# Kernel optimization log

Measured on AMD Instinct MI355X. Metric: run time of the kernel, lower is better.

## Reference

```python
import jax, jax.numpy as jnp
import numpy as np

D_MODEL = 768
D_STATE = 16
D_CONV = 4
EXPAND = 2
D_INNER = EXPAND * D_MODEL          # 1536
DT_RANK = (D_MODEL + 15) // 16      # 48 (mamba default: ceil(d_model/16))


def setup_inputs() -> dict:
    key = jax.random.key(0)
    ks = jax.random.split(key, 8)
    B, T = 2, 1024
    s = 0.02
    return {
        "x": jax.random.normal(ks[0], (B, T, D_MODEL), jnp.float32),
        "ln_g": jnp.ones((D_MODEL,), jnp.float32),
        "ln_b": jnp.zeros((D_MODEL,), jnp.float32),
        "W_in": jax.random.normal(ks[1], (2 * D_INNER, D_MODEL), jnp.float32) * s,
        "conv_w": jax.random.normal(ks[2], (D_INNER, 1, D_CONV), jnp.float32) * s,
        "conv_b": jnp.zeros((D_INNER,), jnp.float32),
        "W_xproj": jax.random.normal(ks[3], (DT_RANK + 2 * D_STATE, D_INNER), jnp.float32) * s,
        "W_dt": jax.random.normal(ks[4], (D_INNER, DT_RANK), jnp.float32) * s,
        "b_dt": jax.random.normal(ks[5], (D_INNER,), jnp.float32) * s,
        "A_log": jnp.log(jnp.broadcast_to(jnp.arange(1.0, D_STATE + 1.0, dtype=jnp.float32), (D_INNER, D_STATE))),
        "Dp": jnp.ones((D_INNER,), jnp.float32),
        "W_out": jax.random.normal(ks[6], (D_MODEL, D_INNER), jnp.float32) * s,
    }


def _mamba_block(x, ln_g, ln_b, W_in, conv_w, conv_b, W_xproj, W_dt, b_dt, A_log, Dp, W_out):
    B, T, D = x.shape
    # LayerNorm
    mu = x.mean(-1, keepdims=True)
    var = ((x - mu) ** 2).mean(-1, keepdims=True)
    h = (x - mu) * jax.lax.rsqrt(var + 1e-5) * ln_g + ln_b
    # in_proj -> [B,T,2*d_inner], split into x-branch and gate z
    xz = h @ W_in.T
    xs, z = jnp.split(xz, 2, axis=-1)
    # causal depthwise conv over time (pad left d_conv-1), then SiLU
    xc = jax.lax.conv_general_dilated(
        xs.transpose(0, 2, 1), conv_w, (1,), [(D_CONV - 1, 0)],
        dimension_numbers=("NCH", "OIH", "NCH"), feature_group_count=D_INNER)
    xc = jax.nn.silu(xc.transpose(0, 2, 1) + conv_b)  # [B,T,d_inner]
    # x_proj -> dt_rank + 2*d_state
    x_dbl = xc @ W_xproj.T
    dt_r = x_dbl[..., :DT_RANK]
    Bm = x_dbl[..., DT_RANK:DT_RANK + D_STATE]       # [B,T,n]
    Cm = x_dbl[..., DT_RANK + D_STATE:]              # [B,T,n]
    dt = jax.nn.softplus(dt_r @ W_dt.T + b_dt)       # [B,T,d_inner]
    A = -jnp.exp(A_log)                              # [d_inner, n]
    dA = jnp.exp(jnp.einsum("btd,dn->btdn", dt, A))  # [B,T,d,n]
    dBu = jnp.einsum("btd,btn->btdn", dt * xc, Bm)   # [B,T,d,n]

    def step(s, inp):
        dA_t, dBu_t, C_t = inp
        s = dA_t * s + dBu_t                          # [B,d,n]
        y_t = jnp.einsum("bdn,bn->bd", s, C_t)
        return s, y_t

    s0 = jnp.zeros((B, D_INNER, D_STATE), x.dtype)
    _, ys = jax.lax.scan(step, s0,
                         (dA.transpose(1, 0, 2, 3), dBu.transpose(1, 0, 2, 3), Cm.transpose(1, 0, 2)))
    y = ys.transpose(1, 0, 2) + Dp * xc              # D skip connection
    y = y * jax.nn.silu(z)                           # gate
    return x + y @ W_out.T                           # out_proj + residual


def reference(x, ln_g, ln_b, W_in, conv_w, conv_b, W_xproj, W_dt, b_dt, A_log, Dp, W_out):
    return _mamba_block(x, ln_g, ln_b, W_in, conv_w, conv_b, W_xproj, W_dt, b_dt, A_log, Dp, W_out)
```

## Files before the change

### kernel.cpp

```cpp
#include <hip/hip_runtime.h>

typedef unsigned short u16;
typedef unsigned int u32;
typedef __attribute__((ext_vector_type(8))) short short8;
typedef __attribute__((ext_vector_type(4))) float f32x4;

#define D_MODEL 768
#define D_INNER 1536
#define D_XZ    3072
#define D_STATE 16
#define DT_RANK 48
#define NROW    2048
#define SEQ     1024
#define XDS     128
#define NCHUNK  128
#define CLEN    8

typedef const __attribute__((address_space(1))) u32 glb_u32;
typedef __attribute__((address_space(3))) u32 lds_u32;

__device__ __forceinline__ float bf2f(u16 u) {
    union { unsigned int i; float f; } v; v.i = ((unsigned int)u) << 16; return v.f;
}
__device__ __forceinline__ u16 f2bf(float f) {
    union { float f; unsigned int i; } v; v.f = f;
    unsigned int r = v.i + 0x7fffu + ((v.i >> 16) & 1u);
    return (u16)(r >> 16);
}
__device__ __forceinline__ void g2lds16(const u16* g, u16* l) {
    __builtin_amdgcn_global_load_lds((glb_u32*)g, (lds_u32*)l, 16, 0, 0);
}

#define N0 (D_XZ * D_MODEL / 4)
#define N1 (D_MODEL * D_INNER / 4)
#define N2 (XDS * D_INNER / 4)
#define N3 (D_INNER * 64 / 4)
#define N4 (D_INNER * D_STATE / 4)
#define N5 (NROW * XDS / 4)
__global__ __launch_bounds__(256) void prep_weights_k(
    const float* __restrict__ W_in, const float* __restrict__ W_out,
    const float* __restrict__ W_xp, const float* __restrict__ W_dt,
    const float* __restrict__ A_log,
    u16* __restrict__ Win_bf, u16* __restrict__ Wout_bf,
    u16* __restrict__ Wxp_bf, u16* __restrict__ Wdt_bf,
    float* __restrict__ negA, float* __restrict__ xdbl)
{
    int gid = blockIdx.x * 256 + threadIdx.x;
    if (gid < N0) {
        float4 v = *(const float4*)(W_in + (size_t)gid * 4);
        u16* o = Win_bf + (size_t)gid * 4;
        o[0]=f2bf(v.x); o[1]=f2bf(v.y); o[2]=f2bf(v.z); o[3]=f2bf(v.w);
    } else if (gid < N0 + N1) {
        int i = gid - N0;
        float4 v = *(const float4*)(W_out + (size_t)i * 4);
        u16* o = Wout_bf + (size_t)i * 4;
        o[0]=f2bf(v.x); o[1]=f2bf(v.y); o[2]=f2bf(v.z); o[3]=f2bf(v.w);
    } else if (gid < N0 + N1 + N2) {
        int i = gid - N0 - N1;
        int n = (i * 4) / D_INNER, k = (i * 4) % D_INNER;
        u16* o = Wxp_bf + (size_t)i * 4;
        if (n < 80) {
            float4 v = *(const float4*)(W_xp + (size_t)n * D_INNER + k);
            o[0]=f2bf(v.x); o[1]=f2bf(v.y); o[2]=f2bf(v.z); o[3]=f2bf(v.w);
        } else { o[0]=0; o[1]=0; o[2]=0; o[3]=0; }
    } else if (gid < N0 + N1 + N2 + N3) {
        int i = gid - N0 - N1 - N2;
        int r = (i * 4) >> 6, c0 = (i * 4) & 63;
        u16* o = Wdt_bf + (size_t)i * 4;
        if (c0 < DT_RANK) {
            float4 v = *(const float4*)(W_dt + (size_t)r * DT_RANK + c0);
            o[0]=f2bf(v.x); o[1]=f2bf(v.y); o[2]=f2bf(v.z); o[3]=f2bf(v.w);
        } else { o[0]=0; o[1]=0; o[2]=0; o[3]=0; }
    } else if (gid < N0 + N1 + N2 + N3 + N4) {
        int i = gid - N0 - N1 - N2 - N3;
        float4 v = *(const float4*)(A_log + (size_t)i * 4);
        float4 o = make_float4(-__expf(v.x), -__expf(v.y), -__expf(v.z), -__expf(v.w));
        *(float4*)(negA + (size_t)i * 4) = o;
    } else if (gid < N0 + N1 + N2 + N3 + N4 + N5) {
        int i = gid - N0 - N1 - N2 - N3 - N4;
        *(float4*)(xdbl + (size_t)i * 4) = make_float4(0.f, 0.f, 0.f, 0.f);
    }
}

__global__ __launch_bounds__(256) void layernorm_k(
    const float* __restrict__ x, const float* __restrict__ g,
    const float* __restrict__ b, u16* __restrict__ h)
{
    int row = blockIdx.x, tid = threadIdx.x;
    const float* xr = x + (size_t)row * D_MODEL;
    float v[3], s = 0.f, sq = 0.f;
#pragma unroll
    for (int j = 0; j < 3; ++j) {
        v[j] = xr[tid + j * 256];
        s += v[j]; sq += v[j] * v[j];
    }
#pragma unroll
    for (int off = 32; off >= 1; off >>= 1) {
        s  += __shfl_xor(s,  off, 64);
        sq += __shfl_xor(sq, off, 64);
    }
    __shared__ float sred[4], sqred[4];
    if ((tid & 63) == 0) { sred[tid >> 6] = s; sqred[tid >> 6] = sq; }
    __syncthreads();
    float st = sred[0] + sred[1] + sred[2] + sred[3];
    float sqt = sqred[0] + sqred[1] + sqred[2] + sqred[3];
    float mu = st * (1.f / D_MODEL);
    float var = sqt * (1.f / D_MODEL) - mu * mu;
    float rstd = rsqrtf(var + 1e-5f);
    u16* hr = h + (size_t)row * D_MODEL;
#pragma unroll
    for (int j = 0; j < 3; ++j) {
        int idx = tid + j * 256;
        hr[idx] = f2bf((v[j] - mu) * rstd * g[idx] + b[idx]);
    }
}

template<int MT, int NT, bool OUT_BF16, bool ADD_RES>
__global__ __launch_bounds__(256) void gemm128(
    const u16* __restrict__ A, const u16* __restrict__ B,
    const float* __restrict__ Res, void* __restrict__ Cv,
    int M, int N, int K)
{
    constexpr int BM = 32 * MT, BN = 32 * NT;
    __shared__ __align__(16) u16 As[BM * 32];
    __shared__ __align__(16) u16 Bs[BN * 32];
    int tid = threadIdx.x, w = tid >> 6, lane = tid & 63;
    int wm = w & 1, wn = w >> 1;
    int m0 = blockIdx.x * BM, n0 = blockIdx.y * BN;
    int mloc = lane & 15, quad = lane >> 4;
    int lr = lane >> 2, lc = lane & 3;
    f32x4 acc[MT][NT] = {};

    for (int k0 = 0; k0 < K; k0 += 32) {
        __syncthreads();
#pragma unroll
        for (int j = w; j < 2 * MT; j += 4) {
            int row = j * 16 + lr;
            int cb = lc ^ ((row >> 1) & 3);
            g2lds16(A + (size_t)(m0 + row) * K + k0 + cb * 8, &As[j * 512]);
        }
#pragma unroll
        for (int j = w; j < 2 * NT; j += 4) {
            int row = j * 16 + lr;
            int cb = lc ^ ((row >> 1) & 3);
            g2lds16(B + (size_t)(n0 + row) * K + k0 + cb * 8, &Bs[j * 512]);
        }
        __syncthreads();
        short8 afr[MT], bfr[NT];
#pragma unroll
        for (int mt = 0; mt < MT; ++mt) {
            int row = wm * MT * 16 + mt * 16 + mloc;
            int cb = quad ^ ((row >> 1) & 3);
            afr[mt] = *(const short8*)(&As[row * 32 + cb * 8]);
        }
#pragma unroll
        for (int nt = 0; nt < NT; ++nt) {
            int row = wn * NT * 16 + nt * 16 + mloc;
            int cb = quad ^ ((row >> 1) & 3);
            bfr[nt] = *(const short8*)(&Bs[row * 32 + cb * 8]);
        }
#pragma unroll
        for (int mt = 0; mt < MT; ++mt)
#pragma unroll
            for (int nt = 0; nt < NT; ++nt)
                acc[mt][nt] = __builtin_amdgcn_mfma_f32_16x16x32_bf16(
                    afr[mt], bfr[nt], acc[mt][nt], 0, 0, 0);
    }
#pragma unroll
    for (int mt = 0; mt < MT; ++mt) {
        int grow0 = m0 + wm * MT * 16 + mt * 16 + quad * 4;
#pragma unroll
        for (int nt = 0; nt < NT; ++nt) {
            int gcol = n0 + wn * NT * 16 + nt * 16 + mloc;
#pragma unroll
            for (int r = 0; r < 4; ++r) {
                size_t idx = (size_t)(grow0 + r) * N + gcol;
                float v = acc[mt][nt][r];
                if (ADD_RES) v += Res[idx];
                if (OUT_BF16) ((u16*)Cv)[idx] = f2bf(v);
                else          ((float*)Cv)[idx] = v;
            }
        }
    }
}

__global__ __launch_bounds__(256) void xproj_splitk(
    const u16* __restrict__ A, const u16* __restrict__ B, float* __restrict__ Cout)
{
    constexpr int MT = 2, NT = 4;
    __shared__ __align__(16) u16 As[64 * 32];
    __shared__ __align__(16) u16 Bs[128 * 32];
    int tid = threadIdx.x, w = tid >> 6, lane = tid & 63;
    int wm = w & 1, wn = w >> 1;
    int m0 = blockIdx.x * 64;
    int kbase = blockIdx.y * 192;
    int mloc = lane & 15, quad = lane >> 4;
    int lr = lane >> 2, lc = lane & 3;
    f32x4 acc[MT][NT] = {};

    for (int k0 = 0; k0 < 192; k0 += 32) {
        __syncthreads();
#pragma unroll
        for (int j = w; j < 2 * MT; j += 4) {
            int row = j * 16 + lr;
            int cb = lc ^ ((row >> 1) & 3);
            g2lds16(A + (size_t)(m0 + row) * D_INNER + kbase + k0 + cb * 8, &As[j * 512]);
        }
#pragma unroll
        for (int j = w; j < 2 * NT; j += 4) {
            int row = j * 16 + lr;
            int cb = lc ^ ((row >> 1) & 3);
            g2lds16(B + (size_t)row * D_INNER + kbase + k0 + cb * 8, &Bs[j * 512]);
        }
        __syncthreads();
        short8 afr[MT], bfr[NT];
#pragma unroll
        for (int mt = 0; mt < MT; ++mt) {
            int row = wm * MT * 16 + mt * 16 + mloc;
            int cb = quad ^ ((row >> 1) & 3);
            afr[mt] = *(const short8*)(&As[row * 32 + cb * 8]);
        }
#pragma unroll
        for (int nt = 0; nt < NT; ++nt) {
            int row = wn * NT * 16 + nt * 16 + mloc;
            int cb = quad ^ ((row >> 1) & 3);
            bfr[nt] = *(const short8*)(&Bs[row * 32 + cb * 8]);
        }
#pragma unroll
        for (int mt = 0; mt < MT; ++mt)
#pragma unroll
            for (int nt = 0; nt < NT; ++nt)
                acc[mt][nt] = __builtin_amdgcn_mfma_f32_16x16x32_bf16(
                    afr[mt], bfr[nt], acc[mt][nt], 0, 0, 0);
    }
#pragma unroll
    for (int mt = 0; mt < MT; ++mt) {
        int grow0 = m0 + wm * MT * 16 + mt * 16 + quad * 4;
#pragma unroll
        for (int nt = 0; nt < NT; ++nt) {
            int gcol = wn * NT * 16 + nt * 16 + mloc;
#pragma unroll
            for (int r = 0; r < 4; ++r)
                unsafeAtomicAdd(&Cout[(size_t)(grow0 + r) * XDS + gcol], acc[mt][nt][r]);
        }
    }
}

__global__ __launch_bounds__(256) void dtgemm_k(
    const float* __restrict__ xdbl, const u16* __restrict__ Wdt,
    const float* __restrict__ bias, u16* __restrict__ dtout)
{
    __shared__ __align__(16) u16 Bs[64 * 72];
    int tid = threadIdx.x, wave = tid >> 6, lane = tid & 63;
    int m0 = blockIdx.x * 64, n0 = blockIdx.y * 64;
    int mloc = lane & 15, quad = lane >> 4;
    {
        int r = tid >> 3, ck = (tid & 7) * 8;
#pragma unroll
        for (int rr = 0; rr < 64; rr += 32) {
            int4 bv = *(const int4*)(Wdt + (size_t)(n0 + r + rr) * 64 + ck);
            *(int4*)(&Bs[(r + rr) * 72 + ck]) = bv;
        }
    }
    int arow = m0 + wave * 16 + mloc;
    const float* ar = xdbl + (size_t)arow * XDS + quad * 8;
    short8 af[2];
#pragma unroll
    for (int h = 0; h < 2; ++h) {
        float4 a0 = *(const float4*)(ar + h * 32);
        float4 a1 = *(const float4*)(ar + h * 32 + 4);
        short8 t;
        t[0]=(short)f2bf(a0.x); t[1]=(short)f2bf(a0.y);
        t[2]=(short)f2bf(a0.z); t[3]=(short)f2bf(a0.w);
        t[4]=(short)f2bf(a1.x); t[5]=(short)f2bf(a1.y);
        t[6]=(short)f2bf(a1.z); t[7]=(short)f2bf(a1.w);
        af[h] = t;
    }
    __syncthreads();
    f32x4 acc[4] = {};
#pragma unroll
    for (int h = 0; h < 2; ++h)
#pragma unroll
        for (int nt = 0; nt < 4; ++nt) {
            short8 bf = *(const short8*)(&Bs[(nt * 16 + mloc) * 72 + h * 32 + quad * 8]);
            acc[nt] = __builtin_amdgcn_mfma_f32_16x16x32_bf16(af[h], bf, acc[nt], 0, 0, 0);
        }
#pragma unroll
    for (int nt = 0; nt < 4; ++nt) {
        int gcol = n0 + nt * 16 + mloc;
        int grow = m0 + wave * 16 + quad * 4;
#pragma unroll
        for (int r = 0; r < 4; ++r) {
            float t = acc[nt][r] + bias[gcol];
            float sp = (t > 15.f) ? t : __logf(1.f + __expf(t));
            dtout[(size_t)(grow + r) * D_INNER + gcol] = f2bf(sp);
        }
    }
}

__global__ __launch_bounds__(256) void conv_silu_k(
    const u16* __restrict__ xz, const float* __restrict__ cw,
    const float* __restrict__ cb, u16* __restrict__ xc)
{
    int gid = blockIdx.x * 256 + threadIdx.x;
    int r = gid / (D_INNER / 4);
    int c4 = (gid - r * (D_INNER / 4)) * 4;
    int t = r & (SEQ - 1);
    float4 cbv = *(const float4*)(cb + c4);
    float acc[4] = {cbv.x, cbv.y, cbv.z, cbv.w};
    float4 wv[4];
#pragma unroll
    for (int j = 0; j < 4; ++j) wv[j] = *(const float4*)(cw + (c4 + j) * 4);
#pragma unroll
    for (int k = 0; k < 4; ++k) {
        int tt = t - 3 + k;
        if (tt >= 0) {
            ushort4 xv = *(const ushort4*)(xz + (size_t)(r - 3 + k) * D_XZ + c4);
            acc[0] += bf2f(xv.x) * ((const float*)&wv[0])[k];
            acc[1] += bf2f(xv.y) * ((const float*)&wv[1])[k];
            acc[2] += bf2f(xv.z) * ((const float*)&wv[2])[k];
            acc[3] += bf2f(xv.w) * ((const float*)&wv[3])[k];
        }
    }
    ushort4 o;
    o.x = f2bf(acc[0] / (1.f + __expf(-acc[0])));
    o.y = f2bf(acc[1] / (1.f + __expf(-acc[1])));
    o.z = f2bf(acc[2] / (1.f + __expf(-acc[2])));
    o.w = f2bf(acc[3] / (1.f + __expf(-acc[3])));
    *(ushort4*)(xc + (size_t)r * D_INNER + c4) = o;
}

__global__ __launch_bounds__(256) void scan_p1(
    const u16* __restrict__ dt, const u16* __restrict__ xc,
    const float* __restrict__ xdbl, const float* __restrict__ negA,
    float* __restrict__ Sbuf, float* __restrict__ dtsumbuf)
{
    __shared__ float Bsh[CLEN][D_STATE];
    int tid = threadIdx.x;
    int gid = blockIdx.x * 256 + tid;
    int d = gid % D_INNER;
    int bcN = gid / D_INNER;
    int c = bcN % NCHUNK, b = bcN / NCHUNK;
    size_t r0 = (size_t)b * SEQ + c * CLEN;
    if (tid < CLEN * D_STATE) {
        int tt = tid >> 4, n = tid & 15;
        Bsh[tt][n] = xdbl[(r0 + tt) * XDS + DT_RANK + n];
    }
    float a[D_STATE], s[D_STATE] = {};
    {
        const float4* Ar = (const float4*)(negA + d * D_STATE);
        float4 a0 = Ar[0], a1 = Ar[1], a2 = Ar[2], a3 = Ar[3];
        a[0]=a0.x; a[1]=a0.y; a[2]=a0.z; a[3]=a0.w;
        a[4]=a1.x; a[5]=a1.y; a[6]=a1.z; a[7]=a1.w;
        a[8]=a2.x; a[9]=a2.y; a[10]=a2.z; a[11]=a2.w;
        a[12]=a3.x; a[13]=a3.y; a[14]=a3.z; a[15]=a3.w;
    }
    float dtv[CLEN], du[CLEN];
    const u16* dp = dt + r0 * D_INNER + d;
    const u16* xp = xc + r0 * D_INNER + d;
#pragma unroll
    for (int t = 0; t < CLEN; ++t) {
        dtv[t] = bf2f(dp[t * D_INNER]);
        du[t] = dtv[t] * bf2f(xp[t * D_INNER]);
    }
    __syncthreads();
    float dtsum = 0.f;
#pragma unroll
    for (int t = 0; t < CLEN; ++t) {
        dtsum += dtv[t];
#pragma unroll
        for (int n = 0; n < D_STATE; ++n)
            s[n] = __expf(dtv[t] * a[n]) * s[n] + du[t] * Bsh[t][n];
    }
    float4* So = (float4*)(Sbuf + (size_t)gid * D_STATE);
#pragma unroll
    for (int j = 0; j < 4; ++j)
        So[j] = make_float4(s[j*4], s[j*4+1], s[j*4+2], s[j*4+3]);
    dtsumbuf[gid] = dtsum;
}

__global__ __launch_bounds__(256) void scan_p2(
    const float* __restrict__ Sbuf, const float* __restrict__ dtsumbuf,
    const float* __restrict__ negA, float* __restrict__ carry)
{
    int gid = blockIdx.x * 256 + threadIdx.x;
    int n = gid % D_STATE;
    int d = (gid / D_STATE) % D_INNER;
    int b = gid / (D_STATE * D_INNER);
    float a = negA[d * D_STATE + n];
    float s = 0.f;
    for (int c = 0; c < NCHUNK; ++c) {
        size_t idx = ((size_t)(b * NCHUNK + c) * D_INNER + d);
        carry[idx * D_STATE + n] = s;
        s = Sbuf[idx * D_STATE + n] + __expf(a * dtsumbuf[idx]) * s;
    }
}

__global__ __launch_bounds__(256) void scan_p3(
    const u16* __restrict__ dt, const u16* __restrict__ xc,
    const u16* __restrict__ xz, const float* __restrict__ xdbl,
    const float* __restrict__ negA, const float* __restrict__ Dp,
    const float* __restrict__ carry, u16* __restrict__ yy)
{
    __shared__ float BCsh[CLEN][2 * D_STATE];
    int tid = threadIdx.x;
    int gid = blockIdx.x * 256 + tid;
    int d = gid % D_INNER;
    int bcN = gid / D_INNER;
    int c = bcN % NCHUNK, b = bcN / NCHUNK;
    size_t r0 = (size_t)b * SEQ + c * CLEN;
    {
        int tt = tid >> 5, j = tid & 31;
        BCsh[tt][j] = xdbl[(r0 + tt) * XDS + DT_RANK + j];
    }
    float a[D_STATE], s[D_STATE];
    {
        const float4* Ci = (const float4*)(carry + (size_t)gid * D_STATE);
        float4 c0 = Ci[0], c1 = Ci[1], c2 = Ci[2], c3 = Ci[3];
        s[0]=c0.x; s[1]=c0.y; s[2]=c0.z; s[3]=c0.w;
        s[4]=c1.x; s[5]=c1.y; s[6]=c1.z; s[7]=c1.w;
        s[8]=c2.x; s[9]=c2.y; s[10]=c2.z; s[11]=c2.w;
        s[12]=c3.x; s[13]=c3.y; s[14]=c3.z; s[15]=c3.w;
        const float4* Ar = (const float4*)(negA + d * D_STATE);
        float4 a0 = Ar[0], a1 = Ar[1], a2 = Ar[2], a3 = Ar[3];
        a[0]=a0.x; a[1]=a0.y; a[2]=a0.z; a[3]=a0.w;
        a[4]=a1.x; a[5]=a1.y; a[6]=a1.z; a[7]=a1.w;
        a[8]=a2.x; a[9]=a2.y; a[10]=a2.z; a[11]=a2.w;
        a[12]=a3.x; a[13]=a3.y; a[14]=a3.z; a[15]=a3.w;
    }
    float dtv[CLEN], xcv[CLEN], zv[CLEN];
    const u16* dp = dt + r0 * D_INNER + d;
    const u16* xp = xc + r0 * D_INNER + d;
    const u16* zp = xz + r0 * D_XZ + D_INNER + d;
#pragma unroll
    for (int t = 0; t < CLEN; ++t) {
        dtv[t] = bf2f(dp[t * D_INNER]);
        xcv[t] = bf2f(xp[t * D_INNER]);
        zv[t]  = bf2f(zp[t * D_XZ]);
    }
    float dpv = Dp[d];
    __syncthreads();
    u16* yp = yy + r0 * D_INNER + d;
#pragma unroll
    for (int t = 0; t < CLEN; ++t) {
        float du = dtv[t] * xcv[t];
        float y = 0.f;
#pragma unroll
        for (int n = 0; n < D_STATE; ++n) {
            s[n] = __expf(dtv[t] * a[n]) * s[n] + du * BCsh[t][n];
            y += s[n] * BCsh[t][D_STATE + n];
        }
        float yv = y + dpv * xcv[t];
        float sig = 1.f / (1.f + __expf(-zv[t]));
        yp[t * D_INNER] = f2bf(yv * (zv[t] * sig));
    }
}

extern "C" void kernel_launch(void* const* d_in, const int* in_sizes, int n_in,
                              void* d_out, int out_size, void* d_ws, size_t ws_size,
                              hipStream_t stream) {
    const float* x      = (const float*)d_in[0];
    const float* ln_g   = (const float*)d_in[1];
    const float* ln_b   = (const float*)d_in[2];
    const float* W_in   = (const float*)d_in[3];
    const float* conv_w = (const float*)d_in[4];
    const float* conv_b = (const float*)d_in[5];
    const float* W_xp   = (const float*)d_in[6];
    const float* W_dt   = (const float*)d_in[7];
    const float* b_dt   = (const float*)d_in[8];
    const float* A_log  = (const float*)d_in[9];
    const float* Dp     = (const float*)d_in[10];
    const float* W_out  = (const float*)d_in[11];
    float* out = (float*)d_out;

    char* ws = (char*)d_ws;
    u16*   h_bf    = (u16*)ws;   ws += (size_t)NROW * D_MODEL * 2;
    u16*   xz_bf   = (u16*)ws;   ws += (size_t)NROW * D_XZ * 2;
    u16*   xc_bf   = (u16*)ws;   ws += (size_t)NROW * D_INNER * 2;
    float* xdbl    = (float*)ws; ws += (size_t)NROW * XDS * 4;
    u16*   dtbuf   = (u16*)ws;   ws += (size_t)NROW * D_INNER * 2;
    u16*   yybuf   = (u16*)ws;   ws += (size_t)NROW * D_INNER * 2;
    u16*   Win_bf  = (u16*)ws;   ws += (size_t)D_XZ * D_MODEL * 2;
    u16*   Wout_bf = (u16*)ws;   ws += (size_t)D_MODEL * D_INNER * 2;
    u16*   Wxp_bf  = (u16*)ws;   ws += (size_t)XDS * D_INNER * 2;
    u16*   Wdt_bf  = (u16*)ws;   ws += (size_t)D_INNER * 64 * 2;
    float* negA    = (float*)ws; ws += (size_t)D_INNER * D_STATE * 4;
    float* Sbuf    = (float*)ws; ws += (size_t)2 * NCHUNK * D_INNER * 16 * 4;
    float* dtsumb  = (float*)ws; ws += (size_t)2 * NCHUNK * D_INNER * 4;
    float* carryb  = (float*)ws;

    prep_weights_k<<<(N0 + N1 + N2 + N3 + N4 + N5 + 255) / 256, 256, 0, stream>>>(
        W_in, W_out, W_xp, W_dt, A_log, Win_bf, Wout_bf, Wxp_bf, Wdt_bf, negA, xdbl);

    layernorm_k<<<NROW, 256, 0, stream>>>(x, ln_g, ln_b, h_bf);
    gemm128<4, 4, true, false><<<dim3(NROW / 128, D_XZ / 128), 256, 0, stream>>>(
        h_bf, Win_bf, nullptr, xz_bf, NROW, D_XZ, D_MODEL);
    conv_silu_k<<<NROW * (D_INNER / 4) / 256, 256, 0, stream>>>(
        xz_bf, conv_w, conv_b, xc_bf);
    xproj_splitk<<<dim3(NROW / 64, 8), 256, 0, stream>>>(xc_bf, Wxp_bf, xdbl);
    dtgemm_k<<<dim3(NROW / 64, D_INNER / 64), 256, 0, stream>>>(
        xdbl, Wdt_bf, b_dt, dtbuf);

    scan_p1<<<2 * NCHUNK * D_INNER / 256, 256, 0, stream>>>(
        dtbuf, xc_bf, xdbl, negA, Sbuf, dtsumb);
    scan_p2<<<2 * D_INNER * D_STATE / 256, 256, 0, stream>>>(
        Sbuf, dtsumb, negA, carryb);
    scan_p3<<<2 * NCHUNK * D_INNER / 256, 256, 0, stream>>>(
        dtbuf, xc_bf, xz_bf, xdbl, negA, Dp, carryb, yybuf);

    gemm128<2, 2, false, true><<<dim3(NROW / 64, D_MODEL / 64), 256, 0, stream>>>(
        yybuf, Wout_bf, x, out, NROW, D_MODEL, D_INNER);
}
```

Measured before the change: 211.8 us.

## Fuse layernorm into prep kernel, split-K out_proj with atomics, retile in_proj

LayerNorm is folded into the weight-prep kernel as extra blocks, and the same launch also zeroes the output buffer. The out_proj GEMM becomes a 2-way split-K kernel that accumulates into the output with atomics, adding the residual in the first slice, to raise block count. The in_proj GEMM tile changes from 128x128 to 128x64, which doubles the grid, and the scan carry loop is unrolled. The cost is a generalized split-K template, extra atomic traffic, and nondeterministic summation order in the output.

```diff
diff --git a/kernel.cpp b/kernel.cpp
--- a/kernel.cpp
+++ b/kernel.cpp
@@ -37,15 +37,51 @@
 #define N3 (D_INNER * 64 / 4)
 #define N4 (D_INNER * D_STATE / 4)
 #define N5 (NROW * XDS / 4)
-__global__ __launch_bounds__(256) void prep_weights_k(
+#define N6 (NROW * D_MODEL / 4)
+#define PREP_BLOCKS ((N0+N1+N2+N3+N4+N5+N6) / 256)
+__global__ __launch_bounds__(256) void prep_ln_k(
+    const float* __restrict__ x, const float* __restrict__ g,
+    const float* __restrict__ bln, u16* __restrict__ h,
     const float* __restrict__ W_in, const float* __restrict__ W_out,
     const float* __restrict__ W_xp, const float* __restrict__ W_dt,
     const float* __restrict__ A_log,
     u16* __restrict__ Win_bf, u16* __restrict__ Wout_bf,
     u16* __restrict__ Wxp_bf, u16* __restrict__ Wdt_bf,
-    float* __restrict__ negA, float* __restrict__ xdbl)
-{
-    int gid = blockIdx.x * 256 + threadIdx.x;
+    float* __restrict__ negA, float* __restrict__ xdbl,
+    float* __restrict__ outz)
+{
+    __shared__ float sred[4], sqred[4];
+    int tid = threadIdx.x;
+    if (blockIdx.x < NROW) {
+        int row = blockIdx.x;
+        const float* xr = x + (size_t)row * D_MODEL;
+        float v[3], s = 0.f, sq = 0.f;
+#pragma unroll
+        for (int j = 0; j < 3; ++j) {
+            v[j] = xr[tid + j * 256];
+            s += v[j]; sq += v[j] * v[j];
+        }
+#pragma unroll
+        for (int off = 32; off >= 1; off >>= 1) {
+            s  += __shfl_xor(s,  off, 64);
+            sq += __shfl_xor(sq, off, 64);
+        }
+        if ((tid & 63) == 0) { sred[tid >> 6] = s; sqred[tid >> 6] = sq; }
+        __syncthreads();
+        float st = sred[0] + sred[1] + sred[2] + sred[3];
+        float sqt = sqred[0] + sqred[1] + sqred[2] + sqred[3];
+        float mu = st * (1.f / D_MODEL);
+        float var = sqt * (1.f / D_MODEL) - mu * mu;
+        float rstd = rsqrtf(var + 1e-5f);
+        u16* hr = h + (size_t)row * D_MODEL;
+#pragma unroll
+        for (int j = 0; j < 3; ++j) {
+            int idx = tid + j * 256;
+            hr[idx] = f2bf((v[j] - mu) * rstd * g[idx] + bln[idx]);
+        }
+        return;
+    }
+    int gid = (blockIdx.x - NROW) * 256 + tid;
     if (gid < N0) {
         float4 v = *(const float4*)(W_in + (size_t)gid * 4);
         u16* o = Win_bf + (size_t)gid * 4;
@@ -74,52 +110,21 @@
     } else if (gid < N0 + N1 + N2 + N3 + N4) {
         int i = gid - N0 - N1 - N2 - N3;
         float4 v = *(const float4*)(A_log + (size_t)i * 4);
-        float4 o = make_float4(-__expf(v.x), -__expf(v.y), -__expf(v.z), -__expf(v.w));
-        *(float4*)(negA + (size_t)i * 4) = o;
+        *(float4*)(negA + (size_t)i * 4) =
+            make_float4(-__expf(v.x), -__expf(v.y), -__expf(v.z), -__expf(v.w));
     } else if (gid < N0 + N1 + N2 + N3 + N4 + N5) {
         int i = gid - N0 - N1 - N2 - N3 - N4;
         *(float4*)(xdbl + (size_t)i * 4) = make_float4(0.f, 0.f, 0.f, 0.f);
-    }
-}
-
-__global__ __launch_bounds__(256) void layernorm_k(
-    const float* __restrict__ x, const float* __restrict__ g,
-    const float* __restrict__ b, u16* __restrict__ h)
-{
-    int row = blockIdx.x, tid = threadIdx.x;
-    const float* xr = x + (size_t)row * D_MODEL;
-    float v[3], s = 0.f, sq = 0.f;
-#pragma unroll
-    for (int j = 0; j < 3; ++j) {
-        v[j] = xr[tid + j * 256];
-        s += v[j]; sq += v[j] * v[j];
-    }
-#pragma unroll
-    for (int off = 32; off >= 1; off >>= 1) {
-        s  += __shfl_xor(s,  off, 64);
-        sq += __shfl_xor(sq, off, 64);
-    }
-    __shared__ float sred[4], sqred[4];
-    if ((tid & 63) == 0) { sred[tid >> 6] = s; sqred[tid >> 6] = sq; }
-    __syncthreads();
-    float st = sred[0] + sred[1] + sred[2] + sred[3];
-    float sqt = sqred[0] + sqred[1] + sqred[2] + sqred[3];
-    float mu = st * (1.f / D_MODEL);
-    float var = sqt * (1.f / D_MODEL) - mu * mu;
-    float rstd = rsqrtf(var + 1e-5f);
-    u16* hr = h + (size_t)row * D_MODEL;
-#pragma unroll
-    for (int j = 0; j < 3; ++j) {
-        int idx = tid + j * 256;
-        hr[idx] = f2bf((v[j] - mu) * rstd * g[idx] + b[idx]);
-    }
-}
-
-template<int MT, int NT, bool OUT_BF16, bool ADD_RES>
+    } else {
+        int i = gid - N0 - N1 - N2 - N3 - N4 - N5;
+        *(float4*)(outz + (size_t)i * 4) = make_float4(0.f, 0.f, 0.f, 0.f);
+    }
+}
+
+template<int MT, int NT, bool OUT_BF16>
 __global__ __launch_bounds__(256) void gemm128(
     const u16* __restrict__ A, const u16* __restrict__ B,
-    const float* __restrict__ Res, void* __restrict__ Cv,
-    int M, int N, int K)
+    void* __restrict__ Cv, int M, int N, int K)
 {
     constexpr int BM = 32 * MT, BN = 32 * NT;
     __shared__ __align__(16) u16 As[BM * 32];
@@ -176,7 +181,6 @@
             for (int r = 0; r < 4; ++r) {
                 size_t idx = (size_t)(grow0 + r) * N + gcol;
                 float v = acc[mt][nt][r];
-                if (ADD_RES) v += Res[idx];
                 if (OUT_BF16) ((u16*)Cv)[idx] = f2bf(v);
                 else          ((float*)Cv)[idx] = v;
             }
@@ -184,33 +188,35 @@
     }
 }
 
-__global__ __launch_bounds__(256) void xproj_splitk(
-    const u16* __restrict__ A, const u16* __restrict__ B, float* __restrict__ Cout)
-{
-    constexpr int MT = 2, NT = 4;
-    __shared__ __align__(16) u16 As[64 * 32];
-    __shared__ __align__(16) u16 Bs[128 * 32];
+template<int MT, int NT, int KSLICE, bool ADD_X>
+__global__ __launch_bounds__(256) void gemm_splitk(
+    const u16* __restrict__ A, const u16* __restrict__ B,
+    const float* __restrict__ X, float* __restrict__ Cout, int K, int CS)
+{
+    constexpr int BM = 32 * MT, BN = 32 * NT;
+    __shared__ __align__(16) u16 As[BM * 32];
+    __shared__ __align__(16) u16 Bs[BN * 32];
     int tid = threadIdx.x, w = tid >> 6, lane = tid & 63;
     int wm = w & 1, wn = w >> 1;
-    int m0 = blockIdx.x * 64;
-    int kbase = blockIdx.y * 192;
+    int m0 = blockIdx.x * BM, n0 = blockIdx.y * BN;
+    int kbase = blockIdx.z * KSLICE;
     int mloc = lane & 15, quad = lane >> 4;
     int lr = lane >> 2, lc = lane & 3;
     f32x4 acc[MT][NT] = {};
 
-    for (int k0 = 0; k0 < 192; k0 += 32) {
+    for (int k0 = 0; k0 < KSLICE; k0 += 32) {
         __syncthreads();
 #pragma unroll
         for (int j = w; j < 2 * MT; j += 4) {
             int row = j * 16 + lr;
             int cb = lc ^ ((row >> 1) & 3);
-            g2lds16(A + (size_t)(m0 + row) * D_INNER + kbase + k0 + cb * 8, &As[j * 512]);
+            g2lds16(A + (size_t)(m0 + row) * K + kbase + k0 + cb * 8, &As[j * 512]);
         }
 #pragma unroll
         for (int j = w; j < 2 * NT; j += 4) {
             int row = j * 16 + lr;
             int cb = lc ^ ((row >> 1) & 3);
-            g2lds16(B + (size_t)row * D_INNER + kbase + k0 + cb * 8, &Bs[j * 512]);
+            g2lds16(B + (size_t)(n0 + row) * K + kbase + k0 + cb * 8, &Bs[j * 512]);
         }
         __syncthreads();
         short8 afr[MT], bfr[NT];
@@ -238,10 +244,14 @@
         int grow0 = m0 + wm * MT * 16 + mt * 16 + quad * 4;
 #pragma unroll
         for (int nt = 0; nt < NT; ++nt) {
-            int gcol = wn * NT * 16 + nt * 16 + mloc;
-#pragma unroll
-            for (int r = 0; r < 4; ++r)
-                unsafeAtomicAdd(&Cout[(size_t)(grow0 + r) * XDS + gcol], acc[mt][nt][r]);
+            int gcol = n0 + wn * NT * 16 + nt * 16 + mloc;
+#pragma unroll
+            for (int r = 0; r < 4; ++r) {
+                size_t idx = (size_t)(grow0 + r) * CS + gcol;
+                float v = acc[mt][nt][r];
+                if (ADD_X && blockIdx.z == 0) v += X[idx];
+                unsafeAtomicAdd(&Cout[idx], v);
+            }
         }
     }
 }
@@ -389,6 +399,7 @@
     int b = gid / (D_STATE * D_INNER);
     float a = negA[d * D_STATE + n];
     float s = 0.f;
+#pragma unroll 8
     for (int c = 0; c < NCHUNK; ++c) {
         size_t idx = ((size_t)(b * NCHUNK + c) * D_INNER + d);
         carry[idx * D_STATE + n] = s;
@@ -489,15 +500,16 @@
     float* dtsumb  = (float*)ws; ws += (size_t)2 * NCHUNK * D_INNER * 4;
     float* carryb  = (float*)ws;
 
-    prep_weights_k<<<(N0 + N1 + N2 + N3 + N4 + N5 + 255) / 256, 256, 0, stream>>>(
-        W_in, W_out, W_xp, W_dt, A_log, Win_bf, Wout_bf, Wxp_bf, Wdt_bf, negA, xdbl);
-
-    layernorm_k<<<NROW, 256, 0, stream>>>(x, ln_g, ln_b, h_bf);
-    gemm128<4, 4, true, false><<<dim3(NROW / 128, D_XZ / 128), 256, 0, stream>>>(
-        h_bf, Win_bf, nullptr, xz_bf, NROW, D_XZ, D_MODEL);
+    prep_ln_k<<<NROW + PREP_BLOCKS, 256, 0, stream>>>(
+        x, ln_g, ln_b, h_bf, W_in, W_out, W_xp, W_dt, A_log,
+        Win_bf, Wout_bf, Wxp_bf, Wdt_bf, negA, xdbl, out);
+
+    gemm128<4, 2, true><<<dim3(NROW / 128, D_XZ / 64), 256, 0, stream>>>(
+        h_bf, Win_bf, xz_bf, NROW, D_XZ, D_MODEL);
     conv_silu_k<<<NROW * (D_INNER / 4) / 256, 256, 0, stream>>>(
         xz_bf, conv_w, conv_b, xc_bf);
-    xproj_splitk<<<dim3(NROW / 64, 8), 256, 0, stream>>>(xc_bf, Wxp_bf, xdbl);
+    gemm_splitk<2, 4, 192, false><<<dim3(NROW / 64, 1, 8), 256, 0, stream>>>(
+        xc_bf, Wxp_bf, nullptr, xdbl, D_INNER, XDS);
     dtgemm_k<<<dim3(NROW / 64, D_INNER / 64), 256, 0, stream>>>(
         xdbl, Wdt_bf, b_dt, dtbuf);
 
@@ -508,6 +520,6 @@
     scan_p3<<<2 * NCHUNK * D_INNER / 256, 256, 0, stream>>>(
         dtbuf, xc_bf, xz_bf, xdbl, negA, Dp, carryb, yybuf);
 
-    gemm128<2, 2, false, true><<<dim3(NROW / 64, D_MODEL / 64), 256, 0, stream>>>(
-        yybuf, Wout_bf, x, out, NROW, D_MODEL, D_INNER);
-}
+    gemm_splitk<2, 2, 768, true><<<dim3(NROW / 64, D_MODEL / 64, 2), 256, 0, stream>>>(
+        yybuf, Wout_bf, x, out, D_INNER, D_MODEL);
+}
```

Result: faster. 206.6 us (-2.5%).
